# Performance work log

Hardware: AMD Instinct MI355X
Metric: run time of the kernel (lower is better)

The kernel has to match this reference:

```python
import jax, jax.numpy as jnp
import numpy as np

B, N, S, C, NS = 2, 20000, 1024, 256, 16
RADIUS, HMIN, HMAX = 0.05, -0.02, 0.04
NA, ND = 12, 4
EPS = 1e-5  # BatchNorm eps


def setup_inputs() -> dict:
    key = jax.random.key(0)
    ks = jax.random.split(key, 40)
    def rn(k, shape, scale=0.05):
        return jax.random.normal(k, shape, jnp.float32) * scale
    inp = {
        "xyz": jax.random.uniform(ks[0], (B, N, 3), jnp.float32),
        "new_xyz": jax.random.uniform(ks[1], (B, S, 3), jnp.float32),
        "view_rot": jax.random.normal(ks[2], (B, S, 3, 3), jnp.float32),
        "features": jax.random.normal(ks[3], (B, C, N), jnp.float32),
    }
    i = 4
    for li, (o, ci) in enumerate([(512, C + 3), (256, 512), (256, 256)], 1):
        inp[f"mlp{li}_w"] = rn(ks[i], (o, ci)); inp[f"mlp{li}_b"] = rn(ks[i + 1], (o,))
        inp[f"mlp{li}_g"] = jnp.ones((o,), jnp.float32) + rn(ks[i + 2], (o,), 0.01)
        inp[f"mlp{li}_be"] = rn(ks[i + 3], (o,)); i += 4
    for name in ("c1", "c2"):
        inp[f"{name}_w"] = rn(ks[i], (256, 256)); inp[f"{name}_b"] = rn(ks[i + 1], (256,))
        inp[f"{name}_g"] = jnp.ones((256,), jnp.float32) + rn(ks[i + 2], (256,), 0.01)
        inp[f"{name}_be"] = rn(ks[i + 3], (256,)); i += 4
    inp["c3_w"] = rn(ks[i], (NA * ND * 2, 256)); inp["c3_b"] = rn(ks[i + 1], (NA * ND * 2,))
    return inp


def _bn(x, g, be):  # eval-mode BatchNorm with running_mean=0, running_var=1
    return x * (g / jnp.sqrt(1.0 + EPS)) + be


def _forward(xyz, new_xyz, view_rot, features,
             mlp1_w, mlp1_b, mlp1_g, mlp1_be,
             mlp2_w, mlp2_b, mlp2_g, mlp2_be,
             mlp3_w, mlp3_b, mlp3_g, mlp3_be,
             c1_w, c1_b, c1_g, c1_be,
             c2_w, c2_b, c2_g, c2_be,
             c3_w, c3_b):
    # ---- cylinder query (CUDA kernel math: r = rot @ (p - c), cylinder axis = x) ----
    # computed per rotation row to keep intermediates at (B,S,N) each
    comp = []
    for i in range(3):
        rw = view_rot[:, :, i, :]  # (B,S,3)
        comp.append(jnp.einsum('bsj,bpj->bsp', rw, xyz) - jnp.sum(rw * new_xyz, -1)[..., None])
    xr, yr, zr = comp  # each (B,S,N)
    mask = (yr * yr + zr * zr < RADIUS * RADIUS) & (xr > HMIN) & (xr < HMAX)
    # first-NS valid indices per seed (ascending), pad with first valid (0 if none)
    vals = jnp.where(mask, jnp.arange(N, dtype=jnp.int32), N)  # (B,S,N)
    neg_top, _ = jax.lax.top_k(-vals, NS)
    idx = -neg_top  # (B,S,NS) ascending
    first = idx[..., :1]
    first = jnp.where(first >= N, 0, first)
    idx = jnp.where(idx >= N, first, idx)
    # ---- group ----
    b_ix = jnp.arange(B)[:, None, None]
    g_xyz = xyz[b_ix, idx]                                  # (B,S,NS,3)
    g_feat = jnp.transpose(features, (0, 2, 1))[b_ix, idx]  # (B,S,NS,C)
    diff = (g_xyz - new_xyz[:, :, None, :]) / RADIUS        # normalize_xyz
    rot_xyz = jnp.einsum('bsnk,bskj->bsnj', diff, view_rot)  # rotate_xyz: diff @ rot
    h = jnp.concatenate([rot_xyz, g_feat], axis=-1)          # (B,S,NS,C+3)
    # ---- SharedMLP (1x1 conv2d + BN + ReLU) ----
    for w, bb, g, be in ((mlp1_w, mlp1_b, mlp1_g, mlp1_be),
                         (mlp2_w, mlp2_b, mlp2_g, mlp2_be),
                         (mlp3_w, mlp3_b, mlp3_g, mlp3_be)):
        h = jax.nn.relu(_bn(jnp.einsum('bsnc,oc->bsno', h, w) + bb, g, be))
    h = h.max(axis=2)  # max-pool over samples -> (B,S,256)
    # ---- pointwise conv1d head ----
    h = jax.nn.relu(_bn(jnp.einsum('bsc,oc->bso', h, c1_w) + c1_b, c1_g, c1_be))
    h = jax.nn.relu(_bn(jnp.einsum('bsc,oc->bso', h, c2_w) + c2_b, c2_g, c2_be))
    out = jnp.einsum('bsc,oc->bso', h, c3_w) + c3_b  # (B,S,NA*ND*2)
    return out


def reference(xyz, new_xyz, view_rot, features,
              mlp1_w, mlp1_b, mlp1_g, mlp1_be,
              mlp2_w, mlp2_b, mlp2_g, mlp2_be,
              mlp3_w, mlp3_b, mlp3_g, mlp3_be,
              c1_w, c1_b, c1_g, c1_be,
              c2_w, c2_b, c2_g, c2_be,
              c3_w, c3_b):
    return _forward(xyz, new_xyz, view_rot, features,
                    mlp1_w, mlp1_b, mlp1_g, mlp1_be,
                    mlp2_w, mlp2_b, mlp2_g, mlp2_be,
                    mlp3_w, mlp3_b, mlp3_g, mlp3_be,
                    c1_w, c1_b, c1_g, c1_be,
                    c2_w, c2_b, c2_g, c2_be,
                    c3_w, c3_b)
```

## Files before the change

kernel.cpp:

```cpp
#include <hip/hip_runtime.h>
#include <hip/hip_bf16.h>
#include <stdint.h>

#define B_   2
#define N_   20000
#define S_   1024
#define C_   256
#define NS_  16
#define NQ   (B_ * S_)
#define M_   (NQ * NS_)
#define K1P  288
#define O1   512
#define O2   256
#define O3   256
#define OUTC 96
#define GRID 16
#define CELLCAP 64
#define MAXCELLS 64

#define R2C   ((float)(0.05 * 0.05))
#define HMINC ((float)(-0.02))
#define HMAXC ((float)(0.04))

__device__ __forceinline__ unsigned short f2b(float f) {
    union { float f; unsigned int i; } x; x.f = f;
    unsigned int r = x.i + 0x7FFFu + ((x.i >> 16) & 1u);
    return (unsigned short)(r >> 16);
}
__device__ __forceinline__ float b2f(unsigned short u) {
    union { unsigned int i; float f; } x; x.i = ((unsigned int)u) << 16; return x.f;
}

__global__ __launch_bounds__(256) void prep_all(const float* __restrict__ m1w,
                                                const float* __restrict__ m2w,
                                                const float* __restrict__ m3w,
                                                unsigned short* __restrict__ w1p,
                                                unsigned short* __restrict__ w2p,
                                                unsigned short* __restrict__ w3p,
                                                int* __restrict__ counts) {
    int i = blockIdx.x * 256 + threadIdx.x;
    if (i < O1 * K1P) {
        int o = i / K1P, k = i - o * K1P;
        float v = 0.0f;
        if (k < 256)      v = m1w[o * 259 + 3 + k];
        else if (k < 259) v = m1w[o * 259 + (k - 256)];
        w1p[i] = (k < 259) ? f2b(v) : (unsigned short)0;
    } else if (i < 278528) {
        int j = i - 147456;
        w2p[j] = f2b(m2w[j]);
    } else if (i < 344064) {
        int j = i - 278528;
        w3p[j] = f2b(m3w[j]);
    } else if (i < 344064 + 2 * GRID * GRID * GRID) {
        counts[i - 344064] = 0;
    }
}

__global__ __launch_bounds__(256) void prep_head_w(const float* __restrict__ c1w,
                                                   const float* __restrict__ c2w,
                                                   const float* __restrict__ c3w,
                                                   unsigned short* __restrict__ c1wb,
                                                   unsigned short* __restrict__ c2wb,
                                                   unsigned short* __restrict__ c3wb) {
    int i = blockIdx.x * 256 + threadIdx.x;
    if (i < 65536) {
        c1wb[i] = f2b(c1w[i]);
    } else if (i < 131072) {
        c2wb[i - 65536] = f2b(c2w[i - 65536]);
    } else if (i < 163840) {
        int j = i - 131072;
        int o = j >> 8, k = j & 255;
        c3wb[j] = (o < OUTC) ? f2b(c3w[o * 256 + k]) : (unsigned short)0;
    }
}

__global__ __launch_bounds__(256) void bin_points(const float* __restrict__ xyz,
                                                  int* __restrict__ counts,
                                                  int4* __restrict__ binned) {
    int i = blockIdx.x * 256 + threadIdx.x;
    if (i >= B_ * N_) return;
    int b = (i >= N_) ? 1 : 0;
    int p = i - b * N_;
    const float* pp = xyz + ((size_t)b * N_ + p) * 3;
    float x = pp[0], y = pp[1], z = pp[2];
    int cx = min(GRID - 1, max(0, (int)(x * GRID)));
    int cy = min(GRID - 1, max(0, (int)(y * GRID)));
    int cz = min(GRID - 1, max(0, (int)(z * GRID)));
    int cell = ((b * GRID + cx) * GRID + cy) * GRID + cz;
    int pos = atomicAdd(&counts[cell], 1);
    if (pos < CELLCAP) {
        int4 e;
        e.x = __float_as_int(x); e.y = __float_as_int(y);
        e.z = __float_as_int(z); e.w = p;
        binned[cell * CELLCAP + pos] = e;
    }
}

__global__ __launch_bounds__(256) void transpose_feat(const float* __restrict__ feat,
                                                      unsigned short* __restrict__ feat_t) {
    __shared__ float tile[32][33];
    int n0 = blockIdx.x * 32, c0 = blockIdx.y * 32, b = blockIdx.z;
    int t = threadIdx.x;
    int nl = t & 31;
#pragma unroll
    for (int i = 0; i < 4; ++i) {
        int cl = (t >> 5) + i * 8;
        tile[cl][nl] = feat[((size_t)(b * C_ + c0 + cl)) * N_ + n0 + nl];
    }
    __syncthreads();
    int nr = t >> 3, c4 = (t & 7) * 4;
    ushort4 v;
    v.x = f2b(tile[c4 + 0][nr]);
    v.y = f2b(tile[c4 + 1][nr]);
    v.z = f2b(tile[c4 + 2][nr]);
    v.w = f2b(tile[c4 + 3][nr]);
    *(ushort4*)(feat_t + ((size_t)(b * N_ + n0 + nr)) * C_ + c0 + c4) = v;
}

__global__ __launch_bounds__(64) void cyl_query_binned(const float* __restrict__ new_xyz,
                                                       const float* __restrict__ view_rot,
                                                       const int* __restrict__ counts,
                                                       const int4* __restrict__ binned,
                                                       int* __restrict__ idx_out,
                                                       int* __restrict__ flags) {
#pragma clang fp contract(off)
    int q = blockIdx.x;
    int b = q >> 10;
    int lane = threadIdx.x;

    __shared__ int pass[64];
    __shared__ int firstv;

    const float* nq = new_xyz + (size_t)q * 3;
    float qx = nq[0], qy = nq[1], qz = nq[2];
    const float* rp = view_rot + (size_t)q * 9;
    float R[9];
#pragma unroll
    for (int i = 0; i < 9; ++i) R[i] = rp[i];
    float dq0 = (R[0]*qx + R[1]*qy) + R[2]*qz;
    float dq1 = (R[3]*qx + R[4]*qy) + R[5]*qz;
    float dq2 = (R[6]*qx + R[7]*qy) + R[8]*qz;

    float a00 = R[4]*R[8] - R[5]*R[7], a01 = R[2]*R[7] - R[1]*R[8], a02 = R[1]*R[5] - R[2]*R[4];
    float a10 = R[5]*R[6] - R[3]*R[8], a11 = R[0]*R[8] - R[2]*R[6], a12 = R[2]*R[3] - R[0]*R[5];
    float a20 = R[3]*R[7] - R[4]*R[6], a21 = R[1]*R[6] - R[0]*R[7], a22 = R[0]*R[4] - R[1]*R[3];
    float det = R[0]*a00 + R[1]*a10 + R[2]*a20;
    float inv = 1.0f / det;
    float lo[3], hi[3];
    const float rho = 0.05f + 1e-3f;
    const float qc[3] = {qx, qy, qz};
    const float ar[3][3] = {{a00,a01,a02},{a10,a11,a12},{a20,a21,a22}};
#pragma unroll
    for (int k = 0; k < 3; ++k) {
        float c0 = ar[k][0] * inv, c1 = ar[k][1] * inv, c2 = ar[k][2] * inv;
        float e0 = c0 * HMINC, e1 = c0 * HMAXC;
        float rr = rho * sqrtf(c1 * c1 + c2 * c2);
        float l = qc[k] + fminf(e0, e1) - rr - 1e-3f;
        float h = qc[k] + fmaxf(e0, e1) + rr + 1e-3f;
        if (!(l > -1e6f && h < 1e6f)) { l = 0.0f; h = 1.0f; }
        lo[k] = l; hi[k] = h;
    }
    int cx0 = max(0, (int)floorf(lo[0] * GRID)), cx1 = min(GRID - 1, (int)floorf(hi[0] * GRID));
    int cy0 = max(0, (int)floorf(lo[1] * GRID)), cy1 = min(GRID - 1, (int)floorf(hi[1] * GRID));
    int cz0 = max(0, (int)floorf(lo[2] * GRID)), cz1 = min(GRID - 1, (int)floorf(hi[2] * GRID));

    int ncells = (cx1 - cx0 + 1) * (cy1 - cy0 + 1) * (cz1 - cz0 + 1);
    if (ncells > MAXCELLS) {
        if (lane == 0) flags[q] = 1;
        return;
    }

    int cnt = 0;
    unsigned long long below_mask = (1ull << lane) - 1ull;

    for (int cx = cx0; cx <= cx1; ++cx)
    for (int cy = cy0; cy <= cy1; ++cy)
    for (int cz = cz0; cz <= cz1; ++cz) {
        int cell = ((b * GRID + cx) * GRID + cy) * GRID + cz;
        int len = counts[cell];
        if (len > CELLCAP) len = CELLCAP;
        bool m = false; int p = 0;
        if (lane < len) {
            int4 e = binned[cell * CELLCAP + lane];
            float px = __int_as_float(e.x), py = __int_as_float(e.y), pz = __int_as_float(e.z);
            p = e.w;
            float xr = ((R[0]*px + R[1]*py) + R[2]*pz) - dq0;
            float yr = ((R[3]*px + R[4]*py) + R[5]*pz) - dq1;
            float zr = ((R[6]*px + R[7]*py) + R[8]*pz) - dq2;
            m = ((yr*yr + zr*zr) < R2C) && (xr > HMINC) && (xr < HMAXC);
        }
        unsigned long long bal = __ballot(m);
        if (bal) {
            int pos = cnt + (int)__popcll(bal & below_mask);
            if (m && pos < 64) pass[pos] = p;
            cnt += (int)__popcll(bal);
        }
    }

    if (cnt > 64) {
        if (lane == 0) flags[q] = 1;
        return;
    }
    if (lane == 0) flags[q] = 0;

    int v = 0x7fffffff;
    if (lane < cnt) v = pass[lane];
    int rank = 0;
    for (int j = 0; j < cnt; ++j) rank += (pass[j] < v) ? 1 : 0;
    if (lane == 0) firstv = 0;
    __syncthreads();
    if (lane < cnt && rank == 0) firstv = v;
    __syncthreads();
    int first = firstv;
    if (lane < cnt && rank < 16) idx_out[q * NS_ + rank] = v;
    if (lane >= cnt && lane < 16) idx_out[q * NS_ + lane] = first;
}

__global__ __launch_bounds__(256) void cyl_query_fallback(const float* __restrict__ xyz,
                                                          const float* __restrict__ new_xyz,
                                                          const float* __restrict__ view_rot,
                                                          const int* __restrict__ flags,
                                                          int* __restrict__ idx_out) {
#pragma clang fp contract(off)
    int q = blockIdx.x;
    if (flags[q] == 0) return;
    int b = q >> 10;
    int t = threadIdx.x;
    int w = t >> 6, lane = t & 63;

    __shared__ int lists[4][NS_];
    __shared__ int cnts[4];

    const float* nq = new_xyz + (size_t)q * 3;
    float qx = nq[0], qy = nq[1], qz = nq[2];
    const float* rp = view_rot + (size_t)q * 9;
    float R[9];
#pragma unroll
    for (int i = 0; i < 9; ++i) R[i] = rp[i];
    float dq0 = (R[0]*qx + R[1]*qy) + R[2]*qz;
    float dq1 = (R[3]*qx + R[4]*qy) + R[5]*qz;
    float dq2 = (R[6]*qx + R[7]*qy) + R[8]*qz;

    int start = w * 5000;
    int end   = min(N_, start + 5000);
    int cnt = 0;
    const float* xb = xyz + (size_t)b * N_ * 3;

    for (int base = start; base < end && cnt < NS_; base += 64) {
        int p = base + lane;
        bool m = false;
        if (p < end) {
            const float* pp = xb + (size_t)p * 3;
            float px = pp[0], py = pp[1], pz = pp[2];
            float xr = ((R[0]*px + R[1]*py) + R[2]*pz) - dq0;
            float yr = ((R[3]*px + R[4]*py) + R[5]*pz) - dq1;
            float zr = ((R[6]*px + R[7]*py) + R[8]*pz) - dq2;
            m = ((yr*yr + zr*zr) < R2C) && (xr > HMINC) && (xr < HMAXC);
        }
        unsigned long long bal = __ballot(m);
        int below = __popcll(bal & ((1ull << lane) - 1ull));
        if (m) {
            int pos = cnt + below;
            if (pos < NS_) lists[w][pos] = p;
        }
        cnt += (int)__popcll(bal);
        if (cnt > NS_) cnt = NS_;
    }
    if (lane == 0) cnts[w] = cnt;
    __syncthreads();

    if (t == 0) {
        int buf[NS_]; int total = 0;
        for (int ww = 0; ww < 4 && total < NS_; ++ww)
            for (int i = 0; i < cnts[ww] && total < NS_; ++i)
                buf[total++] = lists[ww][i];
        int first = (total > 0) ? buf[0] : 0;
        for (int i = 0; i < NS_; ++i)
            idx_out[q * NS_ + i] = (i < total) ? buf[i] : first;
    }
}

__global__ __launch_bounds__(256) void build_h0(const float* __restrict__ xyz,
                                                const float* __restrict__ new_xyz,
                                                const float* __restrict__ view_rot,
                                                const unsigned short* __restrict__ feat_t,
                                                const int* __restrict__ idxs,
                                                unsigned short* __restrict__ h0) {
#pragma clang fp contract(off)
    int q = blockIdx.x;
    int b = q >> 10;
    int t = threadIdx.x;
    __shared__ int pidx[NS_];
    if (t < NS_) pidx[t] = idxs[q * NS_ + t];
    __syncthreads();

#pragma unroll
    for (int pass = 0; pass < 2; ++pass) {
        int n = pass * 8 + (t >> 5);
        int p = pidx[n];
        uint4 v = *(const uint4*)(feat_t + ((size_t)(b * N_ + p)) * C_ + (t & 31) * 8);
        *(uint4*)(h0 + (size_t)(q * NS_ + n) * K1P + (t & 31) * 8) = v;
    }

    if (t < NS_) {
        int n = t, p = pidx[n];
        const float* pp = xyz + ((size_t)b * N_ + p) * 3;
        const float* nq = new_xyz + (size_t)q * 3;
        float dx = (pp[0] - nq[0]) / 0.05f;
        float dy = (pp[1] - nq[1]) / 0.05f;
        float dz = (pp[2] - nq[2]) / 0.05f;
        const float* rp = view_rot + (size_t)q * 9;
        float r0 = (dx * rp[0] + dy * rp[3]) + dz * rp[6];
        float r1 = (dx * rp[1] + dy * rp[4]) + dz * rp[7];
        float r2 = (dx * rp[2] + dy * rp[5]) + dz * rp[8];
        size_t row = (size_t)(q * NS_ + n) * K1P;
        h0[row + 256] = f2b(r0);
        h0[row + 257] = f2b(r1);
        h0[row + 258] = f2b(r2);
    }
    for (int e = t; e < NS_ * 29; e += 256) {
        int n = e / 29, c = 259 + (e - n * 29);
        h0[(size_t)(q * NS_ + n) * K1P + c] = 0;
    }
}

typedef float f32x4 __attribute__((ext_vector_type(4)));
typedef short s16x8 __attribute__((ext_vector_type(8)));

__global__ __launch_bounds__(256) void gemm_bn_relu(const unsigned short* __restrict__ A,
                                                    const unsigned short* __restrict__ W,
                                                    const float* __restrict__ bias,
                                                    const float* __restrict__ gam,
                                                    const float* __restrict__ bet,
                                                    unsigned short* __restrict__ out,
                                                    int M, int Nn, int K) {
    __shared__ __align__(16) unsigned short As[128 * 32];
    __shared__ __align__(16) unsigned short Bs[128 * 32];
    int tid  = threadIdx.x;
    int lane = tid & 63, wave = tid >> 6;
    int m0 = blockIdx.x * 128, n0 = blockIdx.y * 128;
    int wm = (wave >> 1) * 64, wn = (wave & 1) * 64;

    f32x4 acc[4][4] = {};

    for (int k0 = 0; k0 < K; k0 += 32) {
        __syncthreads();
#pragma unroll
        for (int j = 0; j < 2; ++j) {
            int e = j * 256 + tid;
            int r = e >> 2, c8 = (e & 3) << 3;
            *(uint4*)&As[e * 8] = *(const uint4*)(A + (size_t)(m0 + r) * K + k0 + c8);
            *(uint4*)&Bs[e * 8] = *(const uint4*)(W + (size_t)(n0 + r) * K + k0 + c8);
        }
        __syncthreads();

        int kq = (lane >> 4) * 8, rr = lane & 15;
        s16x8 af[4], bfr[4];
#pragma unroll
        for (int i = 0; i < 4; ++i) af[i]  = *(const s16x8*)&As[(wm + i * 16 + rr) * 32 + kq];
#pragma unroll
        for (int j = 0; j < 4; ++j) bfr[j] = *(const s16x8*)&Bs[(wn + j * 16 + rr) * 32 + kq];
#pragma unroll
        for (int i = 0; i < 4; ++i)
#pragma unroll
            for (int j = 0; j < 4; ++j)
                acc[i][j] = __builtin_amdgcn_mfma_f32_16x16x32_bf16(af[i], bfr[j], acc[i][j], 0, 0, 0);
    }

    float inv = 1.0f / sqrtf(1.0f + 1e-5f);
    int col = lane & 15, rq = (lane >> 4) * 4;
#pragma unroll
    for (int j = 0; j < 4; ++j) {
        int n = n0 + wn + j * 16 + col;
        float sc = gam[n] * inv;
        float tb = bias[n] * sc + bet[n];
#pragma unroll
        for (int i = 0; i < 4; ++i) {
            int mbase = m0 + wm + i * 16 + rq;
#pragma unroll
            for (int r = 0; r < 4; ++r) {
                float v = acc[i][j][r] * sc + tb;
                v = fmaxf(v, 0.0f);
                out[(size_t)(mbase + r) * Nn + n] = f2b(v);
            }
        }
    }
}

__global__ __launch_bounds__(256) void gemm_bn_relu_maxpool(const unsigned short* __restrict__ A,
                                                            const unsigned short* __restrict__ W,
                                                            const float* __restrict__ bias,
                                                            const float* __restrict__ gam,
                                                            const float* __restrict__ bet,
                                                            unsigned short* __restrict__ hp,
                                                            int M, int Nn, int K) {
    __shared__ __align__(16) unsigned short As[128 * 32];
    __shared__ __align__(16) unsigned short Bs[128 * 32];
    int tid  = threadIdx.x;
    int lane = tid & 63, wave = tid >> 6;
    int m0 = blockIdx.x * 128, n0 = blockIdx.y * 128;
    int wm = (wave >> 1) * 64, wn = (wave & 1) * 64;

    f32x4 acc[4][4] = {};

    for (int k0 = 0; k0 < K; k0 += 32) {
        __syncthreads();
#pragma unroll
        for (int j = 0; j < 2; ++j) {
            int e = j * 256 + tid;
            int r = e >> 2, c8 = (e & 3) << 3;
            *(uint4*)&As[e * 8] = *(const uint4*)(A + (size_t)(m0 + r) * K + k0 + c8);
            *(uint4*)&Bs[e * 8] = *(const uint4*)(W + (size_t)(n0 + r) * K + k0 + c8);
        }
        __syncthreads();

        int kq = (lane >> 4) * 8, rr = lane & 15;
        s16x8 af[4], bfr[4];
#pragma unroll
        for (int i = 0; i < 4; ++i) af[i]  = *(const s16x8*)&As[(wm + i * 16 + rr) * 32 + kq];
#pragma unroll
        for (int j = 0; j < 4; ++j) bfr[j] = *(const s16x8*)&Bs[(wn + j * 16 + rr) * 32 + kq];
#pragma unroll
        for (int i = 0; i < 4; ++i)
#pragma unroll
            for (int j = 0; j < 4; ++j)
                acc[i][j] = __builtin_amdgcn_mfma_f32_16x16x32_bf16(af[i], bfr[j], acc[i][j], 0, 0, 0);
    }

    float inv = 1.0f / sqrtf(1.0f + 1e-5f);
    int col = lane & 15;
    int qbase = (m0 + wm) >> 4;
#pragma unroll
    for (int j = 0; j < 4; ++j) {
        int n = n0 + wn + j * 16 + col;
        float sc = gam[n] * inv;
        float tb = bias[n] * sc + bet[n];
#pragma unroll
        for (int i = 0; i < 4; ++i) {
            float mx = 0.0f;
#pragma unroll
            for (int r = 0; r < 4; ++r)
                mx = fmaxf(mx, acc[i][j][r] * sc + tb);
            mx = fmaxf(mx, __shfl_xor(mx, 16, 64));
            mx = fmaxf(mx, __shfl_xor(mx, 32, 64));
            if (lane < 16)
                hp[(size_t)(qbase + i) * Nn + n] = f2b(mx);
        }
    }
}

__global__ __launch_bounds__(256) void gemm_c3(const unsigned short* __restrict__ A,
                                               const unsigned short* __restrict__ W,
                                               const float* __restrict__ bias,
                                               float* __restrict__ out,
                                               int M, int K) {
    __shared__ __align__(16) unsigned short As[128 * 32];
    __shared__ __align__(16) unsigned short Bs[128 * 32];
    int tid  = threadIdx.x;
    int lane = tid & 63, wave = tid >> 6;
    int m0 = blockIdx.x * 128;
    int wm = (wave >> 1) * 64, wn = (wave & 1) * 64;

    f32x4 acc[4][4] = {};

    for (int k0 = 0; k0 < K; k0 += 32) {
        __syncthreads();
#pragma unroll
        for (int j = 0; j < 2; ++j) {
            int e = j * 256 + tid;
            int r = e >> 2, c8 = (e & 3) << 3;
            *(uint4*)&As[e * 8] = *(const uint4*)(A + (size_t)(m0 + r) * K + k0 + c8);
            *(uint4*)&Bs[e * 8] = *(const uint4*)(W + (size_t)r * K + k0 + c8);
        }
        __syncthreads();

        int kq = (lane >> 4) * 8, rr = lane & 15;
        s16x8 af[4], bfr[4];
#pragma unroll
        for (int i = 0; i < 4; ++i) af[i]  = *(const s16x8*)&As[(wm + i * 16 + rr) * 32 + kq];
#pragma unroll
        for (int j = 0; j < 4; ++j) bfr[j] = *(const s16x8*)&Bs[(wn + j * 16 + rr) * 32 + kq];
#pragma unroll
        for (int i = 0; i < 4; ++i)
#pragma unroll
            for (int j = 0; j < 4; ++j)
                acc[i][j] = __builtin_amdgcn_mfma_f32_16x16x32_bf16(af[i], bfr[j], acc[i][j], 0, 0, 0);
    }

    int col = lane & 15, rq = (lane >> 4) * 4;
#pragma unroll
    for (int j = 0; j < 4; ++j) {
        int n = wn + j * 16 + col;
        if (n >= OUTC) continue;
        float bb = bias[n];
#pragma unroll
        for (int i = 0; i < 4; ++i) {
            int mbase = m0 + wm + i * 16 + rq;
#pragma unroll
            for (int r = 0; r < 4; ++r)
                out[(size_t)(mbase + r) * OUTC + n] = acc[i][j][r] + bb;
        }
    }
}

extern "C" void kernel_launch(void* const* d_in, const int* in_sizes, int n_in,
                              void* d_out, int out_size, void* d_ws, size_t ws_size,
                              hipStream_t stream) {
    const float* xyz      = (const float*)d_in[0];
    const float* new_xyz  = (const float*)d_in[1];
    const float* view_rot = (const float*)d_in[2];
    const float* feat     = (const float*)d_in[3];
    const float* m1w = (const float*)d_in[4];
    const float* m1b = (const float*)d_in[5];
    const float* m1g = (const float*)d_in[6];
    const float* m1be= (const float*)d_in[7];
    const float* m2w = (const float*)d_in[8];
    const float* m2b = (const float*)d_in[9];
    const float* m2g = (const float*)d_in[10];
    const float* m2be= (const float*)d_in[11];
    const float* m3w = (const float*)d_in[12];
    const float* m3b = (const float*)d_in[13];
    const float* m3g = (const float*)d_in[14];
    const float* m3be= (const float*)d_in[15];
    const float* c1w = (const float*)d_in[16];
    const float* c1b = (const float*)d_in[17];
    const float* c1g = (const float*)d_in[18];
    const float* c1be= (const float*)d_in[19];
    const float* c2w = (const float*)d_in[20];
    const float* c2b = (const float*)d_in[21];
    const float* c2g = (const float*)d_in[22];
    const float* c2be= (const float*)d_in[23];
    const float* c3w = (const float*)d_in[24];
    const float* c3b = (const float*)d_in[25];

    char* ws = (char*)d_ws;
    int*            idxs = (int*)ws;
    unsigned short* w1p  = (unsigned short*)(ws + 131072);
    unsigned short* w2p  = (unsigned short*)(ws + 425984);
    unsigned short* w3p  = (unsigned short*)(ws + 688128);
    unsigned short* h0   = (unsigned short*)(ws + 819200);
    char*           h1b  = ws + 19693568;
    unsigned short* h1   = (unsigned short*)h1b;
    unsigned short* h2   = h0;
    int*            counts = (int*)(h1b + 0);
    int*            flags  = (int*)(h1b + 32768);
    int4*           binned = (int4*)(h1b + 65536);
    unsigned short* featt= (unsigned short*)(h1b + 12582912);
    unsigned short* hp   = (unsigned short*)(h1b + 0);
    unsigned short* g1   = (unsigned short*)(h1b + 4194304);
    unsigned short* g2   = (unsigned short*)(h1b + 8388608);
    unsigned short* c1wb = (unsigned short*)(h1b + 12582912);
    unsigned short* c2wb = (unsigned short*)(h1b + 13631488);
    unsigned short* c3wb = (unsigned short*)(h1b + 14680064);

    hipLaunchKernelGGL(prep_all, dim3((344064 + 8192 + 255) / 256), dim3(256), 0, stream,
                       m1w, m2w, m3w, w1p, w2p, w3p, counts);
    hipLaunchKernelGGL(bin_points, dim3((B_ * N_ + 255) / 256), dim3(256), 0, stream,
                       xyz, counts, binned);
    hipLaunchKernelGGL(cyl_query_binned, dim3(NQ), dim3(64), 0, stream,
                       new_xyz, view_rot, counts, binned, idxs, flags);
    hipLaunchKernelGGL(cyl_query_fallback, dim3(NQ), dim3(256), 0, stream,
                       xyz, new_xyz, view_rot, flags, idxs);
    hipLaunchKernelGGL(transpose_feat, dim3(N_ / 32, C_ / 32, B_), dim3(256), 0, stream, feat, featt);
    hipLaunchKernelGGL(build_h0, dim3(NQ), dim3(256), 0, stream, xyz, new_xyz, view_rot, featt, idxs, h0);
    hipLaunchKernelGGL(gemm_bn_relu, dim3(M_ / 128, O1 / 128), dim3(256), 0, stream,
                       h0, w1p, m1b, m1g, m1be, h1, M_, O1, K1P);
    hipLaunchKernelGGL(gemm_bn_relu, dim3(M_ / 128, O2 / 128), dim3(256), 0, stream,
                       h1, w2p, m2b, m2g, m2be, h2, M_, O2, 512);
    hipLaunchKernelGGL(prep_head_w, dim3(163840 / 256), dim3(256), 0, stream,
                       c1w, c2w, c3w, c1wb, c2wb, c3wb);
    hipLaunchKernelGGL(gemm_bn_relu_maxpool, dim3(M_ / 128, O3 / 128), dim3(256), 0, stream,
                       h2, w3p, m3b, m3g, m3be, hp, M_, O3, 256);
    hipLaunchKernelGGL(gemm_bn_relu, dim3(NQ / 128, 256 / 128), dim3(256), 0, stream,
                       hp, c1wb, c1b, c1g, c1be, g1, NQ, 256, 256);
    hipLaunchKernelGGL(gemm_bn_relu, dim3(NQ / 128, 256 / 128), dim3(256), 0, stream,
                       g1, c2wb, c2b, c2g, c2be, g2, NQ, 256, 256);
    hipLaunchKernelGGL(gemm_c3, dim3(NQ / 128), dim3(256), 0, stream,
                       g2, c3wb, c3b, (float*)d_out, NQ, 256);
}
```

Before: 289.9 us.

## Fuse head conv layers into one kernel and parallelize cylinder query over four waves

The three pointwise head GEMMs (c1, c2, c3) are merged into one kernel that keeps each 128-row intermediate activation tile in shared memory. This removes two launches and the global round-trips for g1 and g2, at the cost of only 16 blocks and a large LDS footprint. The binned cylinder query now uses 256 threads that split the cells across four waves and append hits with shared atomics. It also raises the cell limit to 216 and the candidate capacity to 128, so fewer queries drop into the brute-force fallback.

```diff
diff --git a/kernel.cpp b/kernel.cpp
--- a/kernel.cpp
+++ b/kernel.cpp
@@ -16,7 +16,8 @@
 #define OUTC 96
 #define GRID 16
 #define CELLCAP 64
-#define MAXCELLS 64
+#define MAXCELLS 216
+#define PASSCAP 128
 
 #define R2C   ((float)(0.05 * 0.05))
 #define HMINC ((float)(-0.02))
@@ -117,19 +118,23 @@
     *(ushort4*)(feat_t + ((size_t)(b * N_ + n0 + nr)) * C_ + c0 + c4) = v;
 }
 
-__global__ __launch_bounds__(64) void cyl_query_binned(const float* __restrict__ new_xyz,
-                                                       const float* __restrict__ view_rot,
-                                                       const int* __restrict__ counts,
-                                                       const int4* __restrict__ binned,
-                                                       int* __restrict__ idx_out,
-                                                       int* __restrict__ flags) {
+__global__ __launch_bounds__(256) void cyl_query_binned(const float* __restrict__ new_xyz,
+                                                        const float* __restrict__ view_rot,
+                                                        const int* __restrict__ counts,
+                                                        const int4* __restrict__ binned,
+                                                        int* __restrict__ idx_out,
+                                                        int* __restrict__ flags) {
 #pragma clang fp contract(off)
     int q = blockIdx.x;
     int b = q >> 10;
-    int lane = threadIdx.x;
-
-    __shared__ int pass[64];
+    int tid = threadIdx.x;
+    int wave = tid >> 6, lane = tid & 63;
+
+    __shared__ int pass[PASSCAP];
+    __shared__ int scnt;
     __shared__ int firstv;
+    if (tid == 0) { scnt = 0; firstv = 0; }
+    __syncthreads();
 
     const float* nq = new_xyz + (size_t)q * 3;
     float qx = nq[0], qy = nq[1], qz = nq[2];
@@ -164,56 +169,57 @@
     int cy0 = max(0, (int)floorf(lo[1] * GRID)), cy1 = min(GRID - 1, (int)floorf(hi[1] * GRID));
     int cz0 = max(0, (int)floorf(lo[2] * GRID)), cz1 = min(GRID - 1, (int)floorf(hi[2] * GRID));
 
-    int ncells = (cx1 - cx0 + 1) * (cy1 - cy0 + 1) * (cz1 - cz0 + 1);
+    int nx = cx1 - cx0 + 1, ny = cy1 - cy0 + 1, nz = cz1 - cz0 + 1;
+    int ncells = nx * ny * nz;
     if (ncells > MAXCELLS) {
-        if (lane == 0) flags[q] = 1;
+        if (tid == 0) flags[q] = 1;
         return;
     }
 
-    int cnt = 0;
-    unsigned long long below_mask = (1ull << lane) - 1ull;
-
-    for (int cx = cx0; cx <= cx1; ++cx)
-    for (int cy = cy0; cy <= cy1; ++cy)
-    for (int cz = cz0; cz <= cz1; ++cz) {
+    int nyz = ny * nz;
+    for (int ci = wave; ci < ncells; ci += 4) {
+        int cx = cx0 + ci / nyz;
+        int rem = ci - (ci / nyz) * nyz;
+        int cy = cy0 + rem / nz;
+        int cz = cz0 + rem - (rem / nz) * nz;
         int cell = ((b * GRID + cx) * GRID + cy) * GRID + cz;
         int len = counts[cell];
         if (len > CELLCAP) len = CELLCAP;
-        bool m = false; int p = 0;
         if (lane < len) {
             int4 e = binned[cell * CELLCAP + lane];
             float px = __int_as_float(e.x), py = __int_as_float(e.y), pz = __int_as_float(e.z);
-            p = e.w;
             float xr = ((R[0]*px + R[1]*py) + R[2]*pz) - dq0;
             float yr = ((R[3]*px + R[4]*py) + R[5]*pz) - dq1;
             float zr = ((R[6]*px + R[7]*py) + R[8]*pz) - dq2;
-            m = ((yr*yr + zr*zr) < R2C) && (xr > HMINC) && (xr < HMAXC);
-        }
-        unsigned long long bal = __ballot(m);
-        if (bal) {
-            int pos = cnt + (int)__popcll(bal & below_mask);
-            if (m && pos < 64) pass[pos] = p;
-            cnt += (int)__popcll(bal);
-        }
-    }
-
-    if (cnt > 64) {
-        if (lane == 0) flags[q] = 1;
+            bool m = ((yr*yr + zr*zr) < R2C) && (xr > HMINC) && (xr < HMAXC);
+            if (m) {
+                int pos = atomicAdd(&scnt, 1);
+                if (pos < PASSCAP) pass[pos] = e.w;
+            }
+        }
+    }
+    __syncthreads();
+
+    int cnt = scnt;
+    if (cnt > PASSCAP) {
+        if (tid == 0) flags[q] = 1;
         return;
     }
-    if (lane == 0) flags[q] = 0;
+    if (tid == 0) flags[q] = 0;
 
     int v = 0x7fffffff;
-    if (lane < cnt) v = pass[lane];
-    int rank = 0;
-    for (int j = 0; j < cnt; ++j) rank += (pass[j] < v) ? 1 : 0;
-    if (lane == 0) firstv = 0;
-    __syncthreads();
-    if (lane < cnt && rank == 0) firstv = v;
+    int rank = 0x7fffffff;
+    if (tid < cnt) {
+        v = pass[tid];
+        rank = 0;
+        for (int j = 0; j < cnt; ++j) rank += (pass[j] < v) ? 1 : 0;
+    }
+    __syncthreads();
+    if (rank == 0) firstv = v;
     __syncthreads();
     int first = firstv;
-    if (lane < cnt && rank < 16) idx_out[q * NS_ + rank] = v;
-    if (lane >= cnt && lane < 16) idx_out[q * NS_ + lane] = first;
+    if (rank < 16) idx_out[q * NS_ + rank] = v;
+    if (tid >= cnt && tid < 16) idx_out[q * NS_ + tid] = first;
 }
 
 __global__ __launch_bounds__(256) void cyl_query_fallback(const float* __restrict__ xyz,
@@ -449,56 +455,152 @@
     }
 }
 
-__global__ __launch_bounds__(256) void gemm_c3(const unsigned short* __restrict__ A,
-                                               const unsigned short* __restrict__ W,
-                                               const float* __restrict__ bias,
-                                               float* __restrict__ out,
-                                               int M, int K) {
+__global__ __launch_bounds__(256) void head_fused(const unsigned short* __restrict__ hp,
+                                                  const unsigned short* __restrict__ c1wb,
+                                                  const float* __restrict__ c1b, const float* __restrict__ c1g, const float* __restrict__ c1be,
+                                                  const unsigned short* __restrict__ c2wb,
+                                                  const float* __restrict__ c2b, const float* __restrict__ c2g, const float* __restrict__ c2be,
+                                                  const unsigned short* __restrict__ c3wb,
+                                                  const float* __restrict__ c3b,
+                                                  float* __restrict__ out) {
     __shared__ __align__(16) unsigned short As[128 * 32];
     __shared__ __align__(16) unsigned short Bs[128 * 32];
+    __shared__ __align__(16) unsigned short gbuf[128 * 264];
     int tid  = threadIdx.x;
     int lane = tid & 63, wave = tid >> 6;
     int m0 = blockIdx.x * 128;
     int wm = (wave >> 1) * 64, wn = (wave & 1) * 64;
-
-    f32x4 acc[4][4] = {};
-
-    for (int k0 = 0; k0 < K; k0 += 32) {
+    int kq = (lane >> 4) * 8, rr = lane & 15;
+    int col = lane & 15, rq = (lane >> 4) * 4;
+    float inv = 1.0f / sqrtf(1.0f + 1e-5f);
+
+    {
+        f32x4 acc[2][4][4] = {};
+#pragma unroll
+        for (int nh = 0; nh < 2; ++nh) {
+            for (int k0 = 0; k0 < 256; k0 += 32) {
+                __syncthreads();
+#pragma unroll
+                for (int j = 0; j < 2; ++j) {
+                    int e = j * 256 + tid;
+                    int r = e >> 2, c8 = (e & 3) << 3;
+                    *(uint4*)&As[e * 8] = *(const uint4*)(hp + (size_t)(m0 + r) * 256 + k0 + c8);
+                    *(uint4*)&Bs[e * 8] = *(const uint4*)(c1wb + (size_t)(nh * 128 + r) * 256 + k0 + c8);
+                }
+                __syncthreads();
+                s16x8 af[4], bfr[4];
+#pragma unroll
+                for (int i = 0; i < 4; ++i) af[i]  = *(const s16x8*)&As[(wm + i * 16 + rr) * 32 + kq];
+#pragma unroll
+                for (int j = 0; j < 4; ++j) bfr[j] = *(const s16x8*)&Bs[(wn + j * 16 + rr) * 32 + kq];
+#pragma unroll
+                for (int i = 0; i < 4; ++i)
+#pragma unroll
+                    for (int j = 0; j < 4; ++j)
+                        acc[nh][i][j] = __builtin_amdgcn_mfma_f32_16x16x32_bf16(af[i], bfr[j], acc[nh][i][j], 0, 0, 0);
+            }
+        }
         __syncthreads();
 #pragma unroll
-        for (int j = 0; j < 2; ++j) {
-            int e = j * 256 + tid;
-            int r = e >> 2, c8 = (e & 3) << 3;
-            *(uint4*)&As[e * 8] = *(const uint4*)(A + (size_t)(m0 + r) * K + k0 + c8);
-            *(uint4*)&Bs[e * 8] = *(const uint4*)(W + (size_t)r * K + k0 + c8);
+        for (int nh = 0; nh < 2; ++nh)
+#pragma unroll
+        for (int j = 0; j < 4; ++j) {
+            int n = nh * 128 + wn + j * 16 + col;
+            float sc = c1g[n] * inv;
+            float tb = c1b[n] * sc + c1be[n];
+#pragma unroll
+            for (int i = 0; i < 4; ++i)
+#pragma unroll
+                for (int r = 0; r < 4; ++r) {
+                    int row = wm + i * 16 + rq + r;
+                    gbuf[row * 264 + n] = f2b(fmaxf(acc[nh][i][j][r] * sc + tb, 0.0f));
+                }
+        }
+    }
+    __syncthreads();
+
+    {
+        f32x4 acc[2][4][4] = {};
+#pragma unroll
+        for (int nh = 0; nh < 2; ++nh) {
+            for (int k0 = 0; k0 < 256; k0 += 32) {
+                __syncthreads();
+#pragma unroll
+                for (int j = 0; j < 2; ++j) {
+                    int e = j * 256 + tid;
+                    int r = e >> 2, c8 = (e & 3) << 3;
+                    *(uint4*)&Bs[e * 8] = *(const uint4*)(c2wb + (size_t)(nh * 128 + r) * 256 + k0 + c8);
+                }
+                __syncthreads();
+                s16x8 af[4], bfr[4];
+#pragma unroll
+                for (int i = 0; i < 4; ++i) af[i]  = *(const s16x8*)&gbuf[(wm + i * 16 + rr) * 264 + k0 + kq];
+#pragma unroll
+                for (int j = 0; j < 4; ++j) bfr[j] = *(const s16x8*)&Bs[(wn + j * 16 + rr) * 32 + kq];
+#pragma unroll
+                for (int i = 0; i < 4; ++i)
+#pragma unroll
+                    for (int j = 0; j < 4; ++j)
+                        acc[nh][i][j] = __builtin_amdgcn_mfma_f32_16x16x32_bf16(af[i], bfr[j], acc[nh][i][j], 0, 0, 0);
+            }
         }
         __syncthreads();
-
-        int kq = (lane >> 4) * 8, rr = lane & 15;
-        s16x8 af[4], bfr[4];
-#pragma unroll
-        for (int i = 0; i < 4; ++i) af[i]  = *(const s16x8*)&As[(wm + i * 16 + rr) * 32 + kq];
-#pragma unroll
-        for (int j = 0; j < 4; ++j) bfr[j] = *(const s16x8*)&Bs[(wn + j * 16 + rr) * 32 + kq];
-#pragma unroll
-        for (int i = 0; i < 4; ++i)
-#pragma unroll
-            for (int j = 0; j < 4; ++j)
-                acc[i][j] = __builtin_amdgcn_mfma_f32_16x16x32_bf16(af[i], bfr[j], acc[i][j], 0, 0, 0);
-    }
-
-    int col = lane & 15, rq = (lane >> 4) * 4;
-#pragma unroll
-    for (int j = 0; j < 4; ++j) {
-        int n = wn + j * 16 + col;
-        if (n >= OUTC) continue;
-        float bb = bias[n];
-#pragma unroll
-        for (int i = 0; i < 4; ++i) {
-            int mbase = m0 + wm + i * 16 + rq;
-#pragma unroll
-            for (int r = 0; r < 4; ++r)
-                out[(size_t)(mbase + r) * OUTC + n] = acc[i][j][r] + bb;
+#pragma unroll
+        for (int nh = 0; nh < 2; ++nh)
+#pragma unroll
+        for (int j = 0; j < 4; ++j) {
+            int n = nh * 128 + wn + j * 16 + col;
+            float sc = c2g[n] * inv;
+            float tb = c2b[n] * sc + c2be[n];
+#pragma unroll
+            for (int i = 0; i < 4; ++i)
+#pragma unroll
+                for (int r = 0; r < 4; ++r) {
+                    int row = wm + i * 16 + rq + r;
+                    gbuf[row * 264 + n] = f2b(fmaxf(acc[nh][i][j][r] * sc + tb, 0.0f));
+                }
+        }
+    }
+    __syncthreads();
+
+    {
+        f32x4 acc[4][4] = {};
+        for (int k0 = 0; k0 < 256; k0 += 32) {
+            __syncthreads();
+            {
+                int e = tid;
+#pragma unroll
+                for (int j = 0; j < 2; ++j) {
+                    int ee = j * 256 + tid;
+                    int r = ee >> 2, c8 = (ee & 3) << 3;
+                    *(uint4*)&Bs[ee * 8] = *(const uint4*)(c3wb + (size_t)r * 256 + k0 + c8);
+                }
+                (void)e;
+            }
+            __syncthreads();
+            s16x8 af[4], bfr[4];
+#pragma unroll
+            for (int i = 0; i < 4; ++i) af[i]  = *(const s16x8*)&gbuf[(wm + i * 16 + rr) * 264 + k0 + kq];
+#pragma unroll
+            for (int j = 0; j < 4; ++j) bfr[j] = *(const s16x8*)&Bs[(wn + j * 16 + rr) * 32 + kq];
+#pragma unroll
+            for (int i = 0; i < 4; ++i)
+#pragma unroll
+                for (int j = 0; j < 4; ++j)
+                    acc[i][j] = __builtin_amdgcn_mfma_f32_16x16x32_bf16(af[i], bfr[j], acc[i][j], 0, 0, 0);
+        }
+#pragma unroll
+        for (int j = 0; j < 4; ++j) {
+            int n = wn + j * 16 + col;
+            if (n >= OUTC) continue;
+            float bb = c3b[n];
+#pragma unroll
+            for (int i = 0; i < 4; ++i) {
+                int mbase = m0 + wm + i * 16 + rq;
+#pragma unroll
+                for (int r = 0; r < 4; ++r)
+                    out[(size_t)(mbase + r) * OUTC + n] = acc[i][j][r] + bb;
+            }
         }
     }
 }
@@ -547,8 +649,6 @@
     int4*           binned = (int4*)(h1b + 65536);
     unsigned short* featt= (unsigned short*)(h1b + 12582912);
     unsigned short* hp   = (unsigned short*)(h1b + 0);
-    unsigned short* g1   = (unsigned short*)(h1b + 4194304);
-    unsigned short* g2   = (unsigned short*)(h1b + 8388608);
     unsigned short* c1wb = (unsigned short*)(h1b + 12582912);
     unsigned short* c2wb = (unsigned short*)(h1b + 13631488);
     unsigned short* c3wb = (unsigned short*)(h1b + 14680064);
@@ -557,7 +657,7 @@
                        m1w, m2w, m3w, w1p, w2p, w3p, counts);
     hipLaunchKernelGGL(bin_points, dim3((B_ * N_ + 255) / 256), dim3(256), 0, stream,
                        xyz, counts, binned);
-    hipLaunchKernelGGL(cyl_query_binned, dim3(NQ), dim3(64), 0, stream,
+    hipLaunchKernelGGL(cyl_query_binned, dim3(NQ), dim3(256), 0, stream,
                        new_xyz, view_rot, counts, binned, idxs, flags);
     hipLaunchKernelGGL(cyl_query_fallback, dim3(NQ), dim3(256), 0, stream,
                        xyz, new_xyz, view_rot, flags, idxs);
@@ -571,10 +671,7 @@
                        c1w, c2w, c3w, c1wb, c2wb, c3wb);
     hipLaunchKernelGGL(gemm_bn_relu_maxpool, dim3(M_ / 128, O3 / 128), dim3(256), 0, stream,
                        h2, w3p, m3b, m3g, m3be, hp, M_, O3, 256);
-    hipLaunchKernelGGL(gemm_bn_relu, dim3(NQ / 128, 256 / 128), dim3(256), 0, stream,
-                       hp, c1wb, c1b, c1g, c1be, g1, NQ, 256, 256);
-    hipLaunchKernelGGL(gemm_bn_relu, dim3(NQ / 128, 256 / 128), dim3(256), 0, stream,
-                       g1, c2wb, c2b, c2g, c2be, g2, NQ, 256, 256);
-    hipLaunchKernelGGL(gemm_c3, dim3(NQ / 128), dim3(256), 0, stream,
-                       g2, c3wb, c3b, (float*)d_out, NQ, 256);
-}
+    hipLaunchKernelGGL(head_fused, dim3(NQ / 128), dim3(256), 0, stream,
+                       hp, c1wb, c1b, c1g, c1be, c2wb, c2b, c2g, c2be, c3wb, c3b,
+                       (float*)d_out);
+}
```

Result: slower. 297.5 us (+2.6%).
